# Kernel tuning notes

Measured on AMD Instinct MI355X. Metric: run time of the kernel, lower is better.

The kernel has to match this reference:

```python
import jax, jax.numpy as jnp
import numpy as np

NEG_SLOPE = 0.2  # PyG GATConv leaky_relu slope


def gat_conv(x, src, dst, W, a_src, a_dst, b, concat):
    """PyG-style GATConv (eval mode, self-loops already appended to src/dst).
    x: [N, F_in]; W: [F_in, H*C]; a_src/a_dst: [H, C]; b: [H*C] or [C]."""
    N = x.shape[0]
    H, C = a_src.shape
    h = (x @ W).reshape(N, H, C)                      # [N, H, C]
    e_src = jnp.sum(h * a_src, axis=-1)               # [N, H]
    e_dst = jnp.sum(h * a_dst, axis=-1)               # [N, H]
    e = jax.nn.leaky_relu(e_src[src] + e_dst[dst], NEG_SLOPE)  # [E, H]
    # segment softmax over edges grouped by destination node
    m = jax.ops.segment_max(e, dst, num_segments=N)
    e = jnp.exp(e - m[dst])
    denom = jax.ops.segment_sum(e, dst, num_segments=N)
    alpha = e / (denom[dst] + 1e-16)                  # [E, H]
    msg = h[src] * alpha[..., None]                   # [E, H, C]
    out = jax.ops.segment_sum(msg, dst, num_segments=N)  # [N, H, C]
    out = out.reshape(N, H * C) if concat else out.mean(axis=1)
    return out + b


def setup_inputs() -> dict:
    key = jax.random.key(0)
    N, E = 50000, 800000
    F_in, HID, H, NCLS = 128, 16, 8, 40
    ks = jax.random.split(key, 16)
    glorot = lambda k, shp: jax.random.normal(k, shp, jnp.float32) * np.sqrt(2.0 / (shp[0] + shp[-1]))
    inp = {
        "x": jax.random.normal(ks[0], (N, F_in), jnp.float32),
        "edge_index": jax.random.randint(ks[1], (2, E), 0, N, jnp.int32),
        "W1": glorot(ks[2], (F_in, H * HID)),
        "a1s": glorot(ks[3], (H, HID)),
        "a1d": glorot(ks[4], (H, HID)),
        "b1": jnp.zeros((H * HID,), jnp.float32),
        "W2": glorot(ks[5], (H * HID, H * HID)),
        "a2s": glorot(ks[6], (H, HID)),
        "a2d": glorot(ks[7], (H, HID)),
        "b2": jnp.zeros((H * HID,), jnp.float32),
        "W3": glorot(ks[8], (H * HID, H * NCLS)),
        "a3s": glorot(ks[9], (H, NCLS)),
        "a3d": glorot(ks[10], (H, NCLS)),
        "b3": jnp.zeros((NCLS,), jnp.float32),
    }
    return inp


def reference(x, edge_index, W1, a1s, a1d, b1, W2, a2s, a2d, b2, W3, a3s, a3d, b3):
    N = x.shape[0]
    loops = jnp.arange(N, dtype=edge_index.dtype)
    src = jnp.concatenate([edge_index[0], loops])  # add_self_loops=True
    dst = jnp.concatenate([edge_index[1], loops])
    h = jax.nn.elu(gat_conv(x, src, dst, W1, a1s, a1d, b1, True))
    h = jax.nn.elu(gat_conv(h, src, dst, W2, a2s, a2d, b2, True))
    return gat_conv(h, src, dst, W3, a3s, a3d, b3, False)  # [N, num_classes]
```

## Files before the change

### kernel.cpp

```cpp
#include <hip/hip_runtime.h>
#include <hip/hip_bf16.h>
#include <type_traits>

#define LEAKY 0.2f
#define SC 512

using h2_t = __attribute__((ext_vector_type(2))) _Float16;
using h4_t = __attribute__((ext_vector_type(4))) _Float16;
using f16x8 = __attribute__((ext_vector_type(8))) _Float16;
using f32x4 = __attribute__((ext_vector_type(4))) float;


__global__ __launch_bounds__(256) void count_kernel(const int* __restrict__ ei,
                                                    int* __restrict__ cnt,
                                                    int E, int ET) {
    int e = blockIdx.x * 256 + threadIdx.x;
    if (e >= ET) return;
    int d = (e < E) ? ei[E + e] : (e - E);
    atomicAdd(&cnt[d], 1);
}

__global__ __launch_bounds__(256) void psum_kernel(const int* __restrict__ cnt,
                                                   int* __restrict__ bsum, int N) {
    int b = blockIdx.x, tid = threadIdx.x;
    int base = b * SC;
    int s = 0;
#pragma unroll
    for (int p = 0; p < 2; p++) {
        int i = base + p * 256 + tid;
        if (i < N) s += cnt[i];
    }
#pragma unroll
    for (int m = 1; m < 64; m <<= 1) s += __shfl_xor(s, m);
    __shared__ int ws[4];
    if ((tid & 63) == 0) ws[tid >> 6] = s;
    __syncthreads();
    if (tid == 0) bsum[b] = ws[0] + ws[1] + ws[2] + ws[3];
}

__global__ __launch_bounds__(256) void scanw_kernel(int* __restrict__ cnt,
                                                    const int* __restrict__ bsum,
                                                    int* __restrict__ rowptr,
                                                    int N, int B) {
    int b = blockIdx.x, tid = threadIdx.x;
    int off = 0;
    for (int j = 0; j < b; j++) off += bsum[j];

    __shared__ int lds[256];
    int base = b * SC;
    int i0 = base + 2 * tid, i1 = i0 + 1;
    int v0 = (i0 < N) ? cnt[i0] : 0;
    int v1 = (i1 < N) ? cnt[i1] : 0;
    lds[tid] = v0 + v1;
    __syncthreads();
#pragma unroll
    for (int o = 1; o < 256; o <<= 1) {
        int v = (tid >= o) ? lds[tid - o] : 0;
        __syncthreads();
        lds[tid] += v;
        __syncthreads();
    }
    int excl = (tid == 0) ? 0 : lds[tid - 1];
    int p0 = off + excl;
    int p1 = p0 + v0;
    if (i0 < N) { rowptr[i0] = p0; cnt[i0] = p0; }
    if (i1 < N) { rowptr[i1] = p1; cnt[i1] = p1; }
    if (b == B - 1 && tid == 255) rowptr[N] = off + lds[255];
}

__global__ __launch_bounds__(256) void scatter_kernel(const int* __restrict__ ei,
                                                      int* __restrict__ cursor,
                                                      int* __restrict__ perm,
                                                      int E, int ET) {
    int e = blockIdx.x * 256 + threadIdx.x;
    if (e >= ET) return;
    int s, d;
    if (e < E) { s = ei[e]; d = ei[E + e]; } else { s = e - E; d = s; }
    int pos = atomicAdd(&cursor[d], 1);
    perm[pos] = s;
}


__global__ __launch_bounds__(256) void prep_kernel(const float* __restrict__ x,
                                                   _Float16* __restrict__ xh,
                                                   const float* __restrict__ W1,
                                                   const float* __restrict__ W2,
                                                   const float* __restrict__ W3,
                                                   _Float16* __restrict__ Wt,
                                                   int n4) {
    int i = blockIdx.x * 256 + threadIdx.x;
    if (i < n4) {
        float4 v = ((const float4*)x)[i];
        h4_t o = {(_Float16)v.x, (_Float16)v.y, (_Float16)v.z, (_Float16)v.w};
        ((h4_t*)xh)[i] = o;
        return;
    }
    int j = i - n4;
    if (j >= (128 + 128 + 320) * 128) return;
    if (j < 128 * 128) {
        int n = j >> 7, k = j & 127;
        Wt[j] = (_Float16)W1[k * 128 + n];
    } else if (j < 2 * 128 * 128) {
        int jj = j - 128 * 128;
        int n = jj >> 7, k = jj & 127;
        Wt[j] = (_Float16)W2[k * 128 + n];
    } else {
        int jj = j - 2 * 128 * 128;
        int n = jj >> 7, k = jj & 127;
        Wt[j] = (_Float16)W3[k * 320 + n];
    }
}


template <int C, bool FUSE>
__global__ __launch_bounds__(256) void mgemm_kernel(const _Float16* __restrict__ A,
                                                    const _Float16* __restrict__ Wt,
                                                    const float* __restrict__ As_,
                                                    const float* __restrict__ Ad_,
                                                    _Float16* __restrict__ Hh,
                                                    float* __restrict__ es,
                                                    float* __restrict__ ed,
                                                    int M) {
    constexpr int K = 128;
    constexpr int HC = 8 * C;
    __shared__ __align__(16) unsigned char lds[128 * 128 + 64 * 128];
    unsigned char* Asm = lds;
    unsigned char* Bsm = lds + 128 * 128;

    int tid = threadIdx.x;
    int lane = tid & 63;
    int wid = tid >> 6;
    int wm = wid >> 1, wn = wid & 1;
    int m0 = blockIdx.x * 128, n0 = blockIdx.y * 64;

    f32x4 acc[4][2] = {};

    int fr = lane & 15;
    int fk = lane >> 4;

    for (int k0 = 0; k0 < K; k0 += 64) {
#pragma unroll
        for (int p = 0; p < 4; p++) {
            int g = tid + p * 256;
            int row = g >> 3, kg = g & 7;
            uint4 v = {0, 0, 0, 0};
            int grow = m0 + row;
            if (grow < M) v = *(const uint4*)&A[(size_t)grow * K + k0 + kg * 8];
            *(uint4*)&Asm[row * 128 + ((kg ^ (row & 7)) << 4)] = v;
        }
#pragma unroll
        for (int p = 0; p < 2; p++) {
            int g = tid + p * 256;
            int col = g >> 3, kg = g & 7;
            uint4 v = *(const uint4*)&Wt[(size_t)(n0 + col) * K + k0 + kg * 8];
            *(uint4*)&Bsm[col * 128 + ((kg ^ (col & 7)) << 4)] = v;
        }
        __syncthreads();

#pragma unroll
        for (int kf = 0; kf < 2; kf++) {
            int kg = kf * 4 + fk;
            f16x8 af[4], bf[2];
#pragma unroll
            for (int mf = 0; mf < 4; mf++) {
                int row = wm * 64 + mf * 16 + fr;
                af[mf] = *(f16x8*)&Asm[row * 128 + ((kg ^ (row & 7)) << 4)];
            }
#pragma unroll
            for (int nf = 0; nf < 2; nf++) {
                int col = wn * 32 + nf * 16 + fr;
                bf[nf] = *(f16x8*)&Bsm[col * 128 + ((kg ^ (col & 7)) << 4)];
            }
#pragma unroll
            for (int mf = 0; mf < 4; mf++)
#pragma unroll
                for (int nf = 0; nf < 2; nf++)
                    acc[mf][nf] = __builtin_amdgcn_mfma_f32_16x16x32_f16(
                        af[mf], bf[nf], acc[mf][nf], 0, 0, 0);
        }
        __syncthreads();
    }

    _Float16* Es = (_Float16*)lds;
    int crow = wm * 64 + (lane >> 4) * 4;
    int ccol = wn * 32 + (lane & 15);
#pragma unroll
    for (int mf = 0; mf < 4; mf++)
#pragma unroll
        for (int nf = 0; nf < 2; nf++)
#pragma unroll
            for (int j = 0; j < 4; j++)
                Es[(crow + mf * 16 + j) * 64 + ccol + nf * 16] = (_Float16)acc[mf][nf][j];
    __syncthreads();

#pragma unroll
    for (int p = 0; p < 4; p++) {
        int g = tid + p * 256;
        int row = g >> 3, cg = g & 7;
        int grow = m0 + row;
        if (grow < M)
            *(uint4*)&Hh[(size_t)grow * HC + n0 + cg * 8] = *(uint4*)&Es[row * 64 + cg * 8];
    }

    if constexpr (FUSE) {
#pragma unroll
        for (int p = 0; p < 2; p++) {
            int t = tid + p * 256;
            int row = t >> 2, hq = t & 3;
            int grow = m0 + row;
            int h = (n0 >> 4) + hq;
            const _Float16* rp = &Es[row * 64 + hq * 16];
            const float* ap = &As_[h * 16];
            const float* dp = &Ad_[h * 16];
            float s = 0.f, d = 0.f;
#pragma unroll
            for (int c2 = 0; c2 < 16; c2++) {
                float v = (float)rp[c2];
                s = fmaf(v, ap[c2], s);
                d = fmaf(v, dp[c2], d);
            }
            if (grow < M) {
                es[grow * 8 + h] = s;
                ed[grow * 8 + h] = d;
            }
        }
    }
}


template <int C>
__global__ __launch_bounds__(256) void attn_score_kernel(const _Float16* __restrict__ Hf,
                                                         const float* __restrict__ as_,
                                                         const float* __restrict__ ad_,
                                                         float* __restrict__ es,
                                                         float* __restrict__ ed, int N) {
    int i = blockIdx.x * 256 + threadIdx.x;
    if (i >= N * 8) return;
    int n = i >> 3, h = i & 7;
    const _Float16* hp = Hf + (size_t)n * 8 * C + h * C;
    const float* ap = as_ + h * C;
    const float* bp = ad_ + h * C;
    float s = 0.f, d = 0.f;
#pragma unroll
    for (int c = 0; c < C / 2; c++) {
        h2_t v = *(const h2_t*)&hp[2 * c];
        float v0 = (float)v[0], v1 = (float)v[1];
        s = fmaf(v0, ap[2 * c], s);
        d = fmaf(v0, bp[2 * c], d);
        s = fmaf(v1, ap[2 * c + 1], s);
        d = fmaf(v1, bp[2 * c + 1], d);
    }
    es[i] = s;
    ed[i] = d;
}


template <int C, bool FINAL, typename OutT>
__global__ __launch_bounds__(256) void agg_kernel(const _Float16* __restrict__ Hf,
                                                  const float* __restrict__ es,
                                                  const float* __restrict__ ed,
                                                  const int* __restrict__ rowptr,
                                                  const int* __restrict__ perm,
                                                  const float* __restrict__ bias,
                                                  OutT* __restrict__ Out, int N) {
    constexpr int HC = 8 * C;
    __shared__ float sfeat[FINAL ? 4 : 1][FINAL ? HC : 1];
    int lane = threadIdx.x & 63;
    int wid = threadIdx.x >> 6;
    int d = blockIdx.x * 4 + wid;
    bool active = d < N;
    int start = 0, end = 0;
    if (active) { start = rowptr[d]; end = rowptr[d + 1]; }
    start = __builtin_amdgcn_readfirstlane(start);
    end = __builtin_amdgcn_readfirstlane(end);
    int h8 = lane & 7;
    int eslot = lane >> 3;
    float edh = active ? ed[d * 8 + h8] : 0.f;

    int hh03 = FINAL ? (4 * lane) / C : (2 * lane) / C;
    int hh4 = FINAL ? (256 + lane) / C : 0;

    float acc[FINAL ? 5 : 2];
#pragma unroll
    for (int p = 0; p < (FINAL ? 5 : 2); p++) acc[p] = 0.f;

    float dsum = 0.f;
    for (int q0 = start; q0 < end; q0 += 16) {
        int qq0 = q0 + eslot, qq1 = q0 + 8 + eslot;
        int s_l0 = 0, s_l1 = 0;
        float a_l0 = 0.f, a_l1 = 0.f;
        if (qq0 < end) {
            s_l0 = perm[qq0];
            float v = es[s_l0 * 8 + h8] + edh;
            v = (v >= 0.f) ? v : LEAKY * v;
            a_l0 = __expf(v);
        }
        if (qq1 < end) {
            s_l1 = perm[qq1];
            float v = es[s_l1 * 8 + h8] + edh;
            v = (v >= 0.f) ? v : LEAKY * v;
            a_l1 = __expf(v);
        }
        dsum += a_l0 + a_l1;

        if constexpr (!FINAL) {
            h2_t hv[16];
#pragma unroll
            for (int e = 0; e < 16; e++) {
                int s = (e < 8) ? __builtin_amdgcn_readlane(s_l0, e * 8)
                                : __builtin_amdgcn_readlane(s_l1, (e - 8) * 8);
                hv[e] = *(const h2_t*)&Hf[(size_t)s * HC + 2 * lane];
            }
#pragma unroll
            for (int e = 0; e < 16; e++) {
                float a0 = (e < 8) ? __shfl(a_l0, e * 8 + hh03)
                                   : __shfl(a_l1, (e - 8) * 8 + hh03);
                acc[0] = fmaf(a0, (float)hv[e][0], acc[0]);
                acc[1] = fmaf(a0, (float)hv[e][1], acc[1]);
            }
        } else {
            h4_t hv[16];
            _Float16 hx[16];
#pragma unroll
            for (int e = 0; e < 16; e++) {
                int s = (e < 8) ? __builtin_amdgcn_readlane(s_l0, e * 8)
                                : __builtin_amdgcn_readlane(s_l1, (e - 8) * 8);
                const _Float16* hp = Hf + (size_t)s * HC;
                hv[e] = *(const h4_t*)&hp[4 * lane];
                hx[e] = hp[256 + lane];
            }
#pragma unroll
            for (int e = 0; e < 16; e++) {
                float a03, a4;
                if (e < 8) {
                    a03 = __shfl(a_l0, e * 8 + hh03);
                    a4 = __shfl(a_l0, e * 8 + hh4);
                } else {
                    a03 = __shfl(a_l1, (e - 8) * 8 + hh03);
                    a4 = __shfl(a_l1, (e - 8) * 8 + hh4);
                }
                acc[0] = fmaf(a03, (float)hv[e][0], acc[0]);
                acc[1] = fmaf(a03, (float)hv[e][1], acc[1]);
                acc[2] = fmaf(a03, (float)hv[e][2], acc[2]);
                acc[3] = fmaf(a03, (float)hv[e][3], acc[3]);
                acc[4] = fmaf(a4, (float)hx[e], acc[4]);
            }
        }
    }

#pragma unroll
    for (int m = 8; m < 64; m <<= 1) dsum += __shfl_xor(dsum, m);
    float rden = 1.0f / (dsum + 1e-16f);

    if constexpr (!FINAL) {
        float r0 = __shfl(rden, hh03);
        if (active) {
            float2 bv = *(const float2*)&bias[2 * lane];
            float vx = acc[0] * r0 + bv.x;
            float vy = acc[1] * r0 + bv.y;
            vx = (vx > 0.f) ? vx : expm1f(vx);
            vy = (vy > 0.f) ? vy : expm1f(vy);
            h2_t o = {(_Float16)vx, (_Float16)vy};
            *(h2_t*)&Out[(size_t)d * HC + 2 * lane] = o;
        }
    } else {
        float r03 = __shfl(rden, hh03);
        float r4 = __shfl(rden, hh4);
#pragma unroll
        for (int j = 0; j < 4; j++) sfeat[wid][4 * lane + j] = acc[j] * r03;
        sfeat[wid][256 + lane] = acc[4] * r4;
        __syncthreads();
        if (active && lane < C) {
            float s = 0.f;
#pragma unroll
            for (int h = 0; h < 8; h++) s += sfeat[wid][h * C + lane];
            Out[(size_t)d * C + lane] = s * 0.125f + bias[lane];
        }
    }
}


extern "C" void kernel_launch(void* const* d_in, const int* in_sizes, int n_in,
                              void* d_out, int out_size, void* d_ws, size_t ws_size,
                              hipStream_t stream) {
    const float* x   = (const float*)d_in[0];
    const int*   ei  = (const int*)d_in[1];
    const float* W1  = (const float*)d_in[2];
    const float* a1s = (const float*)d_in[3];
    const float* a1d = (const float*)d_in[4];
    const float* b1  = (const float*)d_in[5];
    const float* W2  = (const float*)d_in[6];
    const float* a2s = (const float*)d_in[7];
    const float* a2d = (const float*)d_in[8];
    const float* b2  = (const float*)d_in[9];
    const float* W3  = (const float*)d_in[10];
    const float* a3s = (const float*)d_in[11];
    const float* a3d = (const float*)d_in[12];
    const float* b3  = (const float*)d_in[13];
    float* out = (float*)d_out;

    const int N = in_sizes[0] / 128;
    const int E = in_sizes[1] / 2;
    const int ET = E + N;
    const int B = (N + SC - 1) / SC;

    char* p = (char*)d_ws;
    _Float16* hbuf = (_Float16*)p; p += (size_t)N * 320 * 2;
    _Float16* xbuf = (_Float16*)p; p += (size_t)N * 128 * 2;
    float* es    = (float*)p; p += (size_t)N * 8 * 4;
    float* edd   = (float*)p; p += (size_t)N * 8 * 4;
    int* cnt     = (int*)p;   p += (size_t)N * 4;
    int* rowptr  = (int*)p;   p += (size_t)(N + 1) * 4;
    int* perm    = (int*)p;   p += (size_t)ET * 4;
    int* bsum    = (int*)p;   p += (size_t)B * 4;
    _Float16* Wt1 = (_Float16*)p; p += 128 * 128 * 2;
    _Float16* Wt2 = (_Float16*)p; p += 128 * 128 * 2;
    _Float16* Wt3 = (_Float16*)p; p += 320 * 128 * 2;

    hipMemsetAsync(cnt, 0, (size_t)N * 4, stream);
    count_kernel<<<(ET + 255) / 256, 256, 0, stream>>>(ei, cnt, E, ET);
    psum_kernel<<<B, 256, 0, stream>>>(cnt, bsum, N);
    scanw_kernel<<<B, 256, 0, stream>>>(cnt, bsum, rowptr, N, B);
    scatter_kernel<<<(ET + 255) / 256, 256, 0, stream>>>(ei, cnt, perm, E, ET);

    int n4 = N * 32;
    int prep_total = n4 + (128 + 128 + 320) * 128;
    prep_kernel<<<(prep_total + 255) / 256, 256, 0, stream>>>(x, xbuf, W1, W2, W3, Wt1, n4);

    int agg_grid = (N + 3) / 4;
    int nh_grid = (N * 8 + 255) / 256;
    int gx = (N + 127) / 128;
    dim3 g128(gx, 2);
    dim3 g320(gx, 5);

    mgemm_kernel<16, true><<<g128, 256, 0, stream>>>(xbuf, Wt1, a1s, a1d, hbuf, es, edd, N);
    agg_kernel<16, false, _Float16><<<agg_grid, 256, 0, stream>>>(hbuf, es, edd, rowptr, perm, b1, xbuf, N);

    mgemm_kernel<16, true><<<g128, 256, 0, stream>>>(xbuf, Wt2, a2s, a2d, hbuf, es, edd, N);
    agg_kernel<16, false, _Float16><<<agg_grid, 256, 0, stream>>>(hbuf, es, edd, rowptr, perm, b2, xbuf, N);

    mgemm_kernel<40, false><<<g320, 256, 0, stream>>>(xbuf, Wt3, nullptr, nullptr, hbuf, nullptr, nullptr, N);
    attn_score_kernel<40><<<nh_grid, 256, 0, stream>>>(hbuf, a3s, a3d, es, edd, N);
    agg_kernel<40, true, float><<<agg_grid, 256, 0, stream>>>(hbuf, es, edd, rowptr, perm, b3, out, N);
}
```

Baseline: 323.1 us.

## Process two destination nodes per wavefront in 16-channel aggregation

The 16-channel aggregation kernel is split out and changed so each 64-lane wavefront handles two destination nodes, one per 32-lane half. Each lane now loads 4 fp16 values per edge row instead of 2, and each iteration covers 8 edges per node. With average degree around 17, the 16-edge chunks left many lanes idle; this aims to cut that waste and the number of loop iterations. The risk is divergence, since both halves iterate to the larger degree of the pair. The final 40-channel kernel is unchanged apart from being de-templated.

```diff
diff --git a/kernel.cpp b/kernel.cpp
--- a/kernel.cpp
+++ b/kernel.cpp
@@ -255,16 +255,104 @@
 }
 
 
-template <int C, bool FINAL, typename OutT>
-__global__ __launch_bounds__(256) void agg_kernel(const _Float16* __restrict__ Hf,
-                                                  const float* __restrict__ es,
-                                                  const float* __restrict__ ed,
-                                                  const int* __restrict__ rowptr,
-                                                  const int* __restrict__ perm,
-                                                  const float* __restrict__ bias,
-                                                  OutT* __restrict__ Out, int N) {
-    constexpr int HC = 8 * C;
-    __shared__ float sfeat[FINAL ? 4 : 1][FINAL ? HC : 1];
+__global__ __launch_bounds__(256) void agg16_kernel(const _Float16* __restrict__ Hf,
+                                                    const float* __restrict__ es,
+                                                    const float* __restrict__ ed,
+                                                    const int* __restrict__ rowptr,
+                                                    const int* __restrict__ perm,
+                                                    const float* __restrict__ bias,
+                                                    _Float16* __restrict__ Out, int N) {
+    int lane = threadIdx.x & 63;
+    int wid = threadIdx.x >> 6;
+    int half = lane >> 5;
+    int l32 = lane & 31;
+    int d = blockIdx.x * 8 + wid * 2 + half;
+    bool active = d < N;
+    int start = 0, end = 0;
+    if (active) { start = rowptr[d]; end = rowptr[d + 1]; }
+    int len = end - start;
+    int lenmax = max(len, __shfl_xor(len, 32));
+    int iters = (lenmax + 7) >> 3;
+
+    int h8 = lane & 7;
+    int eslot = (lane >> 3) & 3;
+    float edh = active ? ed[d * 8 + h8] : 0.f;
+    int hh03 = l32 >> 2;
+
+    float acc0 = 0.f, acc1 = 0.f, acc2 = 0.f, acc3 = 0.f;
+    float dsum = 0.f;
+
+    for (int it = 0; it < iters; ++it) {
+        int q0 = start + it * 8;
+        int qq0 = q0 + eslot, qq1 = q0 + 4 + eslot;
+        int s_l0 = 0, s_l1 = 0;
+        float a_l0 = 0.f, a_l1 = 0.f;
+        if (qq0 < end) {
+            s_l0 = perm[qq0];
+            float v = es[s_l0 * 8 + h8] + edh;
+            v = (v >= 0.f) ? v : LEAKY * v;
+            a_l0 = __expf(v);
+        }
+        if (qq1 < end) {
+            s_l1 = perm[qq1];
+            float v = es[s_l1 * 8 + h8] + edh;
+            v = (v >= 0.f) ? v : LEAKY * v;
+            a_l1 = __expf(v);
+        }
+        dsum += a_l0 + a_l1;
+
+        h4_t hv[8];
+#pragma unroll
+        for (int e = 0; e < 8; e++) {
+            int sA = (e < 4) ? __builtin_amdgcn_readlane(s_l0, e * 8)
+                             : __builtin_amdgcn_readlane(s_l1, (e - 4) * 8);
+            int sB = (e < 4) ? __builtin_amdgcn_readlane(s_l0, 32 + e * 8)
+                             : __builtin_amdgcn_readlane(s_l1, 32 + (e - 4) * 8);
+            int s = half ? sB : sA;
+            hv[e] = *(const h4_t*)&Hf[(size_t)s * 128 + 4 * l32];
+        }
+#pragma unroll
+        for (int e = 0; e < 8; e++) {
+            int bidx = (lane & 32) + (e & 3) * 8 + hh03;
+            float a = (e < 4) ? __shfl(a_l0, bidx) : __shfl(a_l1, bidx);
+            acc0 = fmaf(a, (float)hv[e][0], acc0);
+            acc1 = fmaf(a, (float)hv[e][1], acc1);
+            acc2 = fmaf(a, (float)hv[e][2], acc2);
+            acc3 = fmaf(a, (float)hv[e][3], acc3);
+        }
+    }
+
+    dsum += __shfl_xor(dsum, 8);
+    dsum += __shfl_xor(dsum, 16);
+    float rden = 1.0f / (dsum + 1e-16f);
+    float r = __shfl(rden, (lane & 32) + hh03);
+
+    if (active) {
+        float4 bv = *(const float4*)&bias[4 * l32];
+        float v0 = acc0 * r + bv.x;
+        float v1 = acc1 * r + bv.y;
+        float v2 = acc2 * r + bv.z;
+        float v3 = acc3 * r + bv.w;
+        v0 = (v0 > 0.f) ? v0 : expm1f(v0);
+        v1 = (v1 > 0.f) ? v1 : expm1f(v1);
+        v2 = (v2 > 0.f) ? v2 : expm1f(v2);
+        v3 = (v3 > 0.f) ? v3 : expm1f(v3);
+        h4_t o = {(_Float16)v0, (_Float16)v1, (_Float16)v2, (_Float16)v3};
+        *(h4_t*)&Out[(size_t)d * 128 + 4 * l32] = o;
+    }
+}
+
+
+__global__ __launch_bounds__(256) void agg40_kernel(const _Float16* __restrict__ Hf,
+                                                    const float* __restrict__ es,
+                                                    const float* __restrict__ ed,
+                                                    const int* __restrict__ rowptr,
+                                                    const int* __restrict__ perm,
+                                                    const float* __restrict__ bias,
+                                                    float* __restrict__ Out, int N) {
+    constexpr int C = 40;
+    constexpr int HC = 320;
+    __shared__ float sfeat[4][HC];
     int lane = threadIdx.x & 63;
     int wid = threadIdx.x >> 6;
     int d = blockIdx.x * 4 + wid;
@@ -277,13 +365,10 @@
     int eslot = lane >> 3;
     float edh = active ? ed[d * 8 + h8] : 0.f;
 
-    int hh03 = FINAL ? (4 * lane) / C : (2 * lane) / C;
-    int hh4 = FINAL ? (256 + lane) / C : 0;
-
-    float acc[FINAL ? 5 : 2];
-#pragma unroll
-    for (int p = 0; p < (FINAL ? 5 : 2); p++) acc[p] = 0.f;
-
+    int hh03 = (4 * lane) / C;
+    int hh4 = (256 + lane) / C;
+
+    float acc[5] = {0.f, 0.f, 0.f, 0.f, 0.f};
     float dsum = 0.f;
     for (int q0 = start; q0 < end; q0 += 16) {
         int qq0 = q0 + eslot, qq1 = q0 + 8 + eslot;
@@ -303,48 +388,31 @@
         }
         dsum += a_l0 + a_l1;
 
-        if constexpr (!FINAL) {
-            h2_t hv[16];
-#pragma unroll
-            for (int e = 0; e < 16; e++) {
-                int s = (e < 8) ? __builtin_amdgcn_readlane(s_l0, e * 8)
-                                : __builtin_amdgcn_readlane(s_l1, (e - 8) * 8);
-                hv[e] = *(const h2_t*)&Hf[(size_t)s * HC + 2 * lane];
+        h4_t hv[16];
+        _Float16 hx[16];
+#pragma unroll
+        for (int e = 0; e < 16; e++) {
+            int s = (e < 8) ? __builtin_amdgcn_readlane(s_l0, e * 8)
+                            : __builtin_amdgcn_readlane(s_l1, (e - 8) * 8);
+            const _Float16* hp = Hf + (size_t)s * HC;
+            hv[e] = *(const h4_t*)&hp[4 * lane];
+            hx[e] = hp[256 + lane];
+        }
+#pragma unroll
+        for (int e = 0; e < 16; e++) {
+            float a03, a4;
+            if (e < 8) {
+                a03 = __shfl(a_l0, e * 8 + hh03);
+                a4 = __shfl(a_l0, e * 8 + hh4);
+            } else {
+                a03 = __shfl(a_l1, (e - 8) * 8 + hh03);
+                a4 = __shfl(a_l1, (e - 8) * 8 + hh4);
             }
-#pragma unroll
-            for (int e = 0; e < 16; e++) {
-                float a0 = (e < 8) ? __shfl(a_l0, e * 8 + hh03)
-                                   : __shfl(a_l1, (e - 8) * 8 + hh03);
-                acc[0] = fmaf(a0, (float)hv[e][0], acc[0]);
-                acc[1] = fmaf(a0, (float)hv[e][1], acc[1]);
-            }
-        } else {
-            h4_t hv[16];
-            _Float16 hx[16];
-#pragma unroll
-            for (int e = 0; e < 16; e++) {
-                int s = (e < 8) ? __builtin_amdgcn_readlane(s_l0, e * 8)
-                                : __builtin_amdgcn_readlane(s_l1, (e - 8) * 8);
-                const _Float16* hp = Hf + (size_t)s * HC;
-                hv[e] = *(const h4_t*)&hp[4 * lane];
-                hx[e] = hp[256 + lane];
-            }
-#pragma unroll
-            for (int e = 0; e < 16; e++) {
-                float a03, a4;
-                if (e < 8) {
-                    a03 = __shfl(a_l0, e * 8 + hh03);
-                    a4 = __shfl(a_l0, e * 8 + hh4);
-                } else {
-                    a03 = __shfl(a_l1, (e - 8) * 8 + hh03);
-                    a4 = __shfl(a_l1, (e - 8) * 8 + hh4);
-                }
-                acc[0] = fmaf(a03, (float)hv[e][0], acc[0]);
-                acc[1] = fmaf(a03, (float)hv[e][1], acc[1]);
-                acc[2] = fmaf(a03, (float)hv[e][2], acc[2]);
-                acc[3] = fmaf(a03, (float)hv[e][3], acc[3]);
-                acc[4] = fmaf(a4, (float)hx[e], acc[4]);
-            }
+            acc[0] = fmaf(a03, (float)hv[e][0], acc[0]);
+            acc[1] = fmaf(a03, (float)hv[e][1], acc[1]);
+            acc[2] = fmaf(a03, (float)hv[e][2], acc[2]);
+            acc[3] = fmaf(a03, (float)hv[e][3], acc[3]);
+            acc[4] = fmaf(a4, (float)hx[e], acc[4]);
         }
     }
 
@@ -352,30 +420,17 @@
     for (int m = 8; m < 64; m <<= 1) dsum += __shfl_xor(dsum, m);
     float rden = 1.0f / (dsum + 1e-16f);
 
-    if constexpr (!FINAL) {
-        float r0 = __shfl(rden, hh03);
-        if (active) {
-            float2 bv = *(const float2*)&bias[2 * lane];
-            float vx = acc[0] * r0 + bv.x;
-            float vy = acc[1] * r0 + bv.y;
-            vx = (vx > 0.f) ? vx : expm1f(vx);
-            vy = (vy > 0.f) ? vy : expm1f(vy);
-            h2_t o = {(_Float16)vx, (_Float16)vy};
-            *(h2_t*)&Out[(size_t)d * HC + 2 * lane] = o;
-        }
-    } else {
-        float r03 = __shfl(rden, hh03);
-        float r4 = __shfl(rden, hh4);
-#pragma unroll
-        for (int j = 0; j < 4; j++) sfeat[wid][4 * lane + j] = acc[j] * r03;
-        sfeat[wid][256 + lane] = acc[4] * r4;
-        __syncthreads();
-        if (active && lane < C) {
-            float s = 0.f;
-#pragma unroll
-            for (int h = 0; h < 8; h++) s += sfeat[wid][h * C + lane];
-            Out[(size_t)d * C + lane] = s * 0.125f + bias[lane];
-        }
+    float r03 = __shfl(rden, hh03);
+    float r4 = __shfl(rden, hh4);
+#pragma unroll
+    for (int j = 0; j < 4; j++) sfeat[wid][4 * lane + j] = acc[j] * r03;
+    sfeat[wid][256 + lane] = acc[4] * r4;
+    __syncthreads();
+    if (active && lane < C) {
+        float s = 0.f;
+#pragma unroll
+        for (int h = 0; h < 8; h++) s += sfeat[wid][h * C + lane];
+        Out[(size_t)d * C + lane] = s * 0.125f + bias[lane];
     }
 }
 
@@ -427,19 +482,20 @@
     int prep_total = n4 + (128 + 128 + 320) * 128;
     prep_kernel<<<(prep_total + 255) / 256, 256, 0, stream>>>(x, xbuf, W1, W2, W3, Wt1, n4);
 
-    int agg_grid = (N + 3) / 4;
+    int agg16_grid = (N + 7) / 8;
+    int agg40_grid = (N + 3) / 4;
     int nh_grid = (N * 8 + 255) / 256;
     int gx = (N + 127) / 128;
     dim3 g128(gx, 2);
     dim3 g320(gx, 5);
 
     mgemm_kernel<16, true><<<g128, 256, 0, stream>>>(xbuf, Wt1, a1s, a1d, hbuf, es, edd, N);
-    agg_kernel<16, false, _Float16><<<agg_grid, 256, 0, stream>>>(hbuf, es, edd, rowptr, perm, b1, xbuf, N);
+    agg16_kernel<<<agg16_grid, 256, 0, stream>>>(hbuf, es, edd, rowptr, perm, b1, xbuf, N);
 
     mgemm_kernel<16, true><<<g128, 256, 0, stream>>>(xbuf, Wt2, a2s, a2d, hbuf, es, edd, N);
-    agg_kernel<16, false, _Float16><<<agg_grid, 256, 0, stream>>>(hbuf, es, edd, rowptr, perm, b2, xbuf, N);
+    agg16_kernel<<<agg16_grid, 256, 0, stream>>>(hbuf, es, edd, rowptr, perm, b2, xbuf, N);
 
     mgemm_kernel<40, false><<<g320, 256, 0, stream>>>(xbuf, Wt3, nullptr, nullptr, hbuf, nullptr, nullptr, N);
     attn_score_kernel<40><<<nh_grid, 256, 0, stream>>>(hbuf, a3s, a3d, es, edd, N);
-    agg_kernel<40, true, float><<<agg_grid, 256, 0, stream>>>(hbuf, es, edd, rowptr, perm, b3, out, N);
-}
+    agg40_kernel<<<agg40_grid, 256, 0, stream>>>(hbuf, es, edd, rowptr, perm, b3, out, N);
+}
```

Result: no change. 327.6 us (+1.4%).
